# Kernel tuning notes

Hardware: AMD Instinct MI355X
Metric: run time of the kernel (lower is better)

Reference implementation:

```python
import jax, jax.numpy as jnp
import numpy as np

B, T, C, H = 4, 2048, 1024, 16
D = C // H  # head_dim = 64

def setup_inputs() -> dict:
    key = jax.random.key(0)
    k1, k2, k3 = jax.random.split(key, 3)
    x = jax.random.normal(k1, (B, T, C), dtype=jnp.float32)
    # Linear weights stored as (out_features, in_features) like torch; we apply x @ W.T
    w_attn = jax.random.normal(k2, (3 * C, C), dtype=jnp.float32) * (1.0 / np.sqrt(C))
    w_proj = jax.random.normal(k3, (C, C), dtype=jnp.float32) * (1.0 / np.sqrt(C))
    return {"x": x, "w_attn": w_attn, "w_proj": w_proj}

def reference(x, w_attn, w_proj):
    Bv, Tv, Cv = x.shape
    qkv = jnp.einsum('btc,fc->btf', x, w_attn)  # [B,T,3C]
    q, k, v = jnp.split(qkv, 3, axis=-1)
    # [B,H,T,D]
    q = q.reshape(Bv, Tv, H, D).transpose(0, 2, 1, 3)
    k = k.reshape(Bv, Tv, H, D).transpose(0, 2, 1, 3)
    v = v.reshape(Bv, Tv, H, D).transpose(0, 2, 1, 3)
    scale = 1.0 / np.sqrt(D).astype(np.float32)
    att = jnp.einsum('bhqd,bhkd->bhqk', q, k) * scale
    causal = jnp.tril(jnp.ones((Tv, Tv), dtype=bool))
    att = jnp.where(causal, att, -jnp.inf)
    att = jax.nn.softmax(att, axis=-1)
    y = jnp.einsum('bhqk,bhkd->bhqd', att, v)
    y = y.transpose(0, 2, 1, 3).reshape(Bv, Tv, Cv)
    return jnp.einsum('btc,oc->bto', y, w_proj)
```

## Files before the change

kernel.cpp:

```cpp
#include <hip/hip_runtime.h>
#include <cstdint>
#include <cstddef>

typedef __attribute__((ext_vector_type(8))) short short8;
typedef __attribute__((ext_vector_type(4))) float f32x4;
typedef unsigned int u32;

#define MFMA_BF16(a, b, c) __builtin_amdgcn_mfma_f32_16x16x32_bf16((a), (b), (c), 0, 0, 0)

__device__ __forceinline__ void async16(const void* g, void* l) {
  __builtin_amdgcn_global_load_lds(
      (const __attribute__((address_space(1))) u32*)g,
      (__attribute__((address_space(3))) u32*)l, 16, 0, 0);
}

__device__ __forceinline__ short f2bf(float f) {
  u32 u = __builtin_bit_cast(u32, f);
  u += 0x7fffu + ((u >> 16) & 1u);
  return (short)(u >> 16);
}

__device__ __forceinline__ u32 pack_bf16_trunc(float lo, float hi) {
  return __builtin_amdgcn_perm(__builtin_bit_cast(u32, hi),
                               __builtin_bit_cast(u32, lo), 0x07060302u);
}

__global__ __launch_bounds__(256) void cast_all_kernel(
    const float* __restrict__ x, const float* __restrict__ wa,
    const float* __restrict__ wp, short* __restrict__ xb,
    short* __restrict__ wab, short* __restrict__ wpb) {
  const int i = blockIdx.x * blockDim.x + threadIdx.x;
  const float4* src;
  short4* dst;
  float sc = 1.0f;
  if (i < 2097152) {
    src = (const float4*)x + i;
    dst = (short4*)xb + i;
  } else if (i < 2883584) {
    const int j = i - 2097152;
    if (j < 262144) sc = 0.18033688011112042f;
    src = (const float4*)wa + j;
    dst = (short4*)wab + j;
  } else {
    const int j = i - 2883584;
    src = (const float4*)wp + j;
    dst = (short4*)wpb + j;
  }
  float4 v = *src;
  short4 r;
  r.x = f2bf(v.x * sc); r.y = f2bf(v.y * sc);
  r.z = f2bf(v.z * sc); r.w = f2bf(v.w * sc);
  *dst = r;
}

template <bool OUT_BF16>
__global__ __launch_bounds__(256) void gemm_bt_kernel(
    const short* __restrict__ A, const short* __restrict__ Bt,
    void* __restrict__ Cv, int M, int N, int K) {
  __shared__ __align__(16) short As[128 * 64];
  __shared__ __align__(16) short Bs[128 * 64];

  const int tid  = threadIdx.x;
  const int lane = tid & 63;
  const int wave = tid >> 6;
  const int quad = lane >> 4;
  const int l15  = lane & 15;

  const int id  = blockIdx.y * gridDim.x + blockIdx.x;
  const int xcd = id & 7;
  const int j   = id >> 3;
  const int by  = xcd * 8 + (j & 7);
  const int bx  = j >> 3;
  const int bm  = by * 128;
  const int bn  = bx * 128;

  const int wm = (wave >> 1) * 64;
  const int wn = (wave & 1) * 64;

  f32x4 acc[4][4];
#pragma unroll
  for (int i = 0; i < 4; ++i)
#pragma unroll
    for (int jj = 0; jj < 4; ++jj) acc[i][jj] = (f32x4){0.f, 0.f, 0.f, 0.f};

  int srow[4], scol[4];
#pragma unroll
  for (int it = 0; it < 4; ++it) {
    const int s = tid + it * 256;
    srow[it] = s >> 3;
    scol[it] = ((s & 7) ^ (srow[it] & 7)) * 8;
  }
  const int xk = l15 & 7;

  for (int k0 = 0; k0 < K; k0 += 64) {
    __syncthreads();
#pragma unroll
    for (int it = 0; it < 4; ++it) {
      const int s = tid + it * 256;
      async16(A  + (size_t)(bm + srow[it]) * K + k0 + scol[it], &As[s * 8]);
      async16(Bt + (size_t)(bn + srow[it]) * K + k0 + scol[it], &Bs[s * 8]);
    }
    __syncthreads();

    short8 af[4][2], bf[4][2];
#pragma unroll
    for (int mt = 0; mt < 4; ++mt) {
      const int ra = (wm + mt * 16 + l15) * 64;
      af[mt][0] = *(const short8*)&As[ra + ((quad) ^ xk) * 8];
      af[mt][1] = *(const short8*)&As[ra + ((4 + quad) ^ xk) * 8];
    }
#pragma unroll
    for (int nt = 0; nt < 4; ++nt) {
      const int rb = (wn + nt * 16 + l15) * 64;
      bf[nt][0] = *(const short8*)&Bs[rb + ((quad) ^ xk) * 8];
      bf[nt][1] = *(const short8*)&Bs[rb + ((4 + quad) ^ xk) * 8];
    }
#pragma unroll
    for (int kk = 0; kk < 2; ++kk)
#pragma unroll
      for (int mt = 0; mt < 4; ++mt)
#pragma unroll
        for (int nt = 0; nt < 4; ++nt)
          acc[mt][nt] = MFMA_BF16(af[mt][kk], bf[nt][kk], acc[mt][nt]);
  }

#pragma unroll
  for (int mt = 0; mt < 4; ++mt) {
    const int r0e = bm + wm + mt * 16 + quad * 4;
#pragma unroll
    for (int nt = 0; nt < 4; ++nt) {
      const int c = bn + wn + nt * 16 + l15;
#pragma unroll
      for (int reg = 0; reg < 4; ++reg) {
        float v = acc[mt][nt][reg];
        if (OUT_BF16)
          ((short*)Cv)[(size_t)(r0e + reg) * N + c] = f2bf(v);
        else
          ((float*)Cv)[(size_t)(r0e + reg) * N + c] = v;
      }
    }
  }
}

__global__ __launch_bounds__(256) void vtrans_kernel(
    const short* __restrict__ qkv, short* __restrict__ vt2) {
  __shared__ __align__(16) short Ts[64 * 80];
  const int kt = blockIdx.x;
  const int t0 = kt * 64;
  const int bh = blockIdx.y;
  const int b = bh >> 4, h = bh & 15;
  const int tid = threadIdx.x;
#pragma unroll
  for (int it = 0; it < 2; ++it) {
    const int ci = tid + it * 256;
    const int t = ci >> 3, cw = ci & 7;
    short8 v = *(const short8*)(qkv + (size_t)(b * 2048 + t0 + t) * 3072 +
                                2048 + h * 64 + cw * 8);
    *(short8*)&Ts[t * 80 + cw * 8] = v;
  }
  __syncthreads();
#pragma unroll
  for (int it = 0; it < 2; ++it) {
    const int ci = tid + it * 256;
    const int d = ci >> 3, c2 = ci & 7;
    short tmp[8];
#pragma unroll
    for (int j = 0; j < 8; ++j) tmp[j] = Ts[(c2 * 8 + j) * 80 + d];
    short* dst = vt2 +
        (size_t)((bh * 32 + kt) * 8 + (d >> 4) * 2 + (c2 >> 2)) * 512 +
        ((c2 & 3) * 16 + (d & 15)) * 8;
    *(short8*)dst = *(short8*)tmp;
  }
}

__global__ __launch_bounds__(256, 4) void attn_kernel(
    const short* __restrict__ qkv, const short* __restrict__ vt2,
    short* __restrict__ y) {
  __shared__ __align__(16) short Ks[2][4096];
  __shared__ __align__(16) short Ps[4][1024];

  const int bh    = blockIdx.x;
  const int pairi = blockIdx.y;
  const int b = bh >> 4, h = bh & 15;
  const int tid  = threadIdx.x;
  const int lane = tid & 63;
  const int wave = tid >> 6;
  const int quad = lane >> 4, l15 = lane & 15;
  const int base_row = b * 2048;
  short* Pw = &Ps[wave][0];

  const int s0 = tid, s1 = tid + 256;
  const int r0s = s0 >> 3, c0s = (s0 & 7) ^ (r0s & 7);
  const int r1s = s1 >> 3, c1s = (s1 & 7) ^ (r1s & 7);
  const short* kbase0 = qkv + (size_t)(base_row + r0s) * 3072 + 1024 + h * 64 + c0s * 8;
  const short* kbase1 = qkv + (size_t)(base_row + r1s) * 3072 + 1024 + h * 64 + c1s * 8;

  const short* v2base = vt2 + (size_t)bh * 32 * 4096 + (size_t)lane * 8;

  const int xk = l15 & 7;

  for (int half = 0; half < 2; ++half) {
    const int qi  = half ? (31 - pairi) : pairi;
    const int nkt = qi + 1;
    const int qg0 = qi * 64 + wave * 16;

    short8 qf[2];
    {
      const short* qp = qkv +
          (size_t)(base_row + qg0 + l15) * 3072 + h * 64 + quad * 8;
      qf[0] = *(const short8*)qp;
      qf[1] = *(const short8*)(qp + 32);
    }
    float l_r = 0.f;
    f32x4 o[4];
#pragma unroll
    for (int dt = 0; dt < 4; ++dt) o[dt] = (f32x4){0.f, 0.f, 0.f, 0.f};

    async16(kbase0, &Ks[0][s0 * 8]);
    async16(kbase1, &Ks[0][s1 * 8]);

    for (int kt = 0; kt < nkt; ++kt) {
      const int kvb = kt * 64;
      __syncthreads();

      if (kt + 1 < nkt) {
        const int nb = (kt + 1) & 1;
        const size_t koff = (size_t)(kvb + 64) * 3072;
        async16(kbase0 + koff, &Ks[nb][s0 * 8]);
        async16(kbase1 + koff, &Ks[nb][s1 * 8]);
      }
      const short* Kb = &Ks[kt & 1][0];

      const short* vp = v2base + (size_t)kt * 4096;
      short8 vf[4][2];
#pragma unroll
      for (int dt = 0; dt < 4; ++dt) {
        vf[dt][0] = *(const short8*)(vp + (dt * 2 + 0) * 512);
        vf[dt][1] = *(const short8*)(vp + (dt * 2 + 1) * 512);
      }

      short8 kf[4][2];
#pragma unroll
      for (int nt = 0; nt < 4; ++nt) {
        kf[nt][0] = *(const short8*)&Kb[(nt * 16 + l15) * 64 + ((quad) ^ xk) * 8];
        kf[nt][1] = *(const short8*)&Kb[(nt * 16 + l15) * 64 + ((4 + quad) ^ xk) * 8];
      }

      f32x4 s[4];
#pragma unroll
      for (int nt = 0; nt < 4; ++nt) {
        s[nt] = MFMA_BF16(kf[nt][0], qf[0], ((f32x4){0.f, 0.f, 0.f, 0.f}));
        s[nt] = MFMA_BF16(kf[nt][1], qf[1], s[nt]);
      }

      float p[4][4];
      if (kvb + 64 <= qg0) {
#pragma unroll
        for (int nt = 0; nt < 4; ++nt)
#pragma unroll
          for (int r = 0; r < 4; ++r)
            p[nt][r] = __builtin_amdgcn_exp2f(s[nt][r]);
      } else {
        const int qrel = qg0 + l15 - kvb;
#pragma unroll
        for (int nt = 0; nt < 4; ++nt)
#pragma unroll
          for (int r = 0; r < 4; ++r) {
            const int kvl = nt * 16 + quad * 4 + r;
            p[nt][r] = (kvl <= qrel) ? __builtin_amdgcn_exp2f(s[nt][r]) : 0.f;
          }
      }

      float rs = ((p[0][0] + p[0][1]) + (p[0][2] + p[0][3])) +
                 ((p[1][0] + p[1][1]) + (p[1][2] + p[1][3])) +
                 ((p[2][0] + p[2][1]) + (p[2][2] + p[2][3])) +
                 ((p[3][0] + p[3][1]) + (p[3][2] + p[3][3]));
      rs += __shfl_xor(rs, 16);
      rs += __shfl_xor(rs, 32);
      l_r += rs;

#pragma unroll
      for (int nt = 0; nt < 4; ++nt) {
        u32 w0 = pack_bf16_trunc(p[nt][0], p[nt][1]);
        u32 w1 = pack_bf16_trunc(p[nt][2], p[nt][3]);
        const int p0 = 8 * nt + 2 * quad;
        u32* dst = (u32*)Pw + (p0 >> 4) * 256 + ((p0 >> 2) & 3) * 64 +
                   l15 * 4 + (p0 & 3);
        *(uint2*)dst = make_uint2(w0, w1);
      }
      short8 pf0 = *(const short8*)&Pw[quad * 128 + l15 * 8];
      short8 pf1 = *(const short8*)&Pw[512 + quad * 128 + l15 * 8];

#pragma unroll
      for (int dt = 0; dt < 4; ++dt) {
        o[dt] = MFMA_BF16(vf[dt][0], pf0, o[dt]);
        o[dt] = MFMA_BF16(vf[dt][1], pf1, o[dt]);
      }
    }

    {
      const float inv = 1.f / l_r;
#pragma unroll
      for (int dt = 0; dt < 4; ++dt) {
        const int d = dt * 16 + quad * 4;
        u32 w0 = pack_bf16_trunc(o[dt][0] * inv, o[dt][1] * inv);
        u32 w1 = pack_bf16_trunc(o[dt][2] * inv, o[dt][3] * inv);
        *(uint2*)&Pw[(d >> 5) * 512 + l15 * 32 + (d & 31)] = make_uint2(w0, w1);
      }
      const int qq = lane >> 2, ck = lane & 3;
      const size_t yrow = (size_t)(base_row + qg0 + qq);
#pragma unroll
      for (int kkd = 0; kkd < 2; ++kkd) {
        short8 vv = *(const short8*)&Pw[kkd * 512 + qq * 32 + ck * 8];
        *(short8*)(y + yrow * 1024 + h * 64 + kkd * 32 + ck * 8) = vv;
      }
    }
    __syncthreads();
  }
}

extern "C" void kernel_launch(void* const* d_in, const int* in_sizes, int n_in,
                              void* d_out, int out_size, void* d_ws,
                              size_t ws_size, hipStream_t stream) {
  const float* x  = (const float*)d_in[0];
  const float* wa = (const float*)d_in[1];
  const float* wp = (const float*)d_in[2];
  float* out = (float*)d_out;

  char* ws = (char*)d_ws;
  short* xb  = (short*)(ws + 0);
  short* wab = (short*)(ws + 16777216);
  short* wpb = (short*)(ws + 23068672);
  short* qkv = (short*)(ws + 25165824);
  short* yb  = (short*)(ws + 75497472);
  short* vtb = xb;

  cast_all_kernel<<<12288, 256, 0, stream>>>(x, wa, wp, xb, wab, wpb);

  gemm_bt_kernel<true><<<dim3(3072 / 128, 8192 / 128), 256, 0, stream>>>(
      xb, wab, (void*)qkv, 8192, 3072, 1024);

  vtrans_kernel<<<dim3(32, 64), 256, 0, stream>>>(qkv, vtb);

  attn_kernel<<<dim3(64, 16), 256, 0, stream>>>(qkv, vtb, yb);

  gemm_bt_kernel<false><<<dim3(1024 / 128, 8192 / 128), 256, 0, stream>>>(
      yb, wpb, (void*)out, 8192, 1024, 1024);
}
```

Before: 242.2 us.

## Fuse V transpose into QKV GEMM epilogue and drop vtrans kernel

The QKV GEMM epilogue now writes the V columns directly in the MFMA-fragment transposed layout inside the qkv buffer's V region, packing four bf16 values per 8-byte store. This removes the separate vtrans kernel launch and its extra read/write pass over V. The attention kernel reads V fragments from the re-laid-out qkv region with a 3072-element row stride. The cost is scattered 8-byte stores in the GEMM epilogue and V loads in attention that stride across rows, which may coalesce worse than the old contiguous vt2 buffer.

```diff
diff --git a/kernel.cpp b/kernel.cpp
--- a/kernel.cpp
+++ b/kernel.cpp
@@ -53,7 +53,7 @@
   *dst = r;
 }
 
-template <bool OUT_BF16>
+template <bool OUT_BF16, bool V_FUSE>
 __global__ __launch_bounds__(256) void gemm_bt_kernel(
     const short* __restrict__ A, const short* __restrict__ Bt,
     void* __restrict__ Cv, int M, int N, int K) {
@@ -124,58 +124,54 @@
           acc[mt][nt] = MFMA_BF16(af[mt][kk], bf[nt][kk], acc[mt][nt]);
   }
 
-#pragma unroll
-  for (int mt = 0; mt < 4; ++mt) {
-    const int r0e = bm + wm + mt * 16 + quad * 4;
-#pragma unroll
-    for (int nt = 0; nt < 4; ++nt) {
-      const int c = bn + wn + nt * 16 + l15;
-#pragma unroll
-      for (int reg = 0; reg < 4; ++reg) {
-        float v = acc[mt][nt][reg];
-        if (OUT_BF16)
-          ((short*)Cv)[(size_t)(r0e + reg) * N + c] = f2bf(v);
-        else
-          ((float*)Cv)[(size_t)(r0e + reg) * N + c] = v;
-      }
-    }
-  }
-}
-
-__global__ __launch_bounds__(256) void vtrans_kernel(
-    const short* __restrict__ qkv, short* __restrict__ vt2) {
-  __shared__ __align__(16) short Ts[64 * 80];
-  const int kt = blockIdx.x;
-  const int t0 = kt * 64;
-  const int bh = blockIdx.y;
-  const int b = bh >> 4, h = bh & 15;
-  const int tid = threadIdx.x;
-#pragma unroll
-  for (int it = 0; it < 2; ++it) {
-    const int ci = tid + it * 256;
-    const int t = ci >> 3, cw = ci & 7;
-    short8 v = *(const short8*)(qkv + (size_t)(b * 2048 + t0 + t) * 3072 +
-                                2048 + h * 64 + cw * 8);
-    *(short8*)&Ts[t * 80 + cw * 8] = v;
-  }
-  __syncthreads();
-#pragma unroll
-  for (int it = 0; it < 2; ++it) {
-    const int ci = tid + it * 256;
-    const int d = ci >> 3, c2 = ci & 7;
-    short tmp[8];
-#pragma unroll
-    for (int j = 0; j < 8; ++j) tmp[j] = Ts[(c2 * 8 + j) * 80 + d];
-    short* dst = vt2 +
-        (size_t)((bh * 32 + kt) * 8 + (d >> 4) * 2 + (c2 >> 2)) * 512 +
-        ((c2 & 3) * 16 + (d & 15)) * 8;
-    *(short8*)dst = *(short8*)tmp;
+  if (V_FUSE && bn >= 2048) {
+    const int b   = bm >> 11;
+    const int btt = bm & 2047;
+#pragma unroll
+    for (int mt = 0; mt < 4; ++mt) {
+      const int tt   = btt + wm + mt * 16;
+      const int kt   = tt >> 6;
+      const int t64b = (tt & 63) + quad * 4;
+      const int kkb  = t64b >> 5;
+      const int q16  = (t64b >> 3) & 3;
+      const int jb   = t64b & 7;
+#pragma unroll
+      for (int nt = 0; nt < 4; ++nt) {
+        const int dcol = bn - 2048 + wn + nt * 16;
+        const int h  = dcol >> 6;
+        const int dt = (dcol >> 4) & 3;
+        short* dst = (short*)Cv +
+            (size_t)(b * 2048 + kt * 64 + h * 4 + dt) * 3072 + 2048 +
+            kkb * 512 + (q16 * 16 + l15) * 8 + jb;
+        u32 w0 = (u32)(unsigned short)f2bf(acc[mt][nt][0]) |
+                 ((u32)(unsigned short)f2bf(acc[mt][nt][1]) << 16);
+        u32 w1 = (u32)(unsigned short)f2bf(acc[mt][nt][2]) |
+                 ((u32)(unsigned short)f2bf(acc[mt][nt][3]) << 16);
+        *(uint2*)dst = make_uint2(w0, w1);
+      }
+    }
+  } else {
+#pragma unroll
+    for (int mt = 0; mt < 4; ++mt) {
+      const int r0e = bm + wm + mt * 16 + quad * 4;
+#pragma unroll
+      for (int nt = 0; nt < 4; ++nt) {
+        const int c = bn + wn + nt * 16 + l15;
+#pragma unroll
+        for (int reg = 0; reg < 4; ++reg) {
+          float v = acc[mt][nt][reg];
+          if (OUT_BF16)
+            ((short*)Cv)[(size_t)(r0e + reg) * N + c] = f2bf(v);
+          else
+            ((float*)Cv)[(size_t)(r0e + reg) * N + c] = v;
+        }
+      }
+    }
   }
 }
 
 __global__ __launch_bounds__(256, 4) void attn_kernel(
-    const short* __restrict__ qkv, const short* __restrict__ vt2,
-    short* __restrict__ y) {
+    const short* __restrict__ qkv, short* __restrict__ y) {
   __shared__ __align__(16) short Ks[2][4096];
   __shared__ __align__(16) short Ps[4][1024];
 
@@ -195,7 +191,8 @@
   const short* kbase0 = qkv + (size_t)(base_row + r0s) * 3072 + 1024 + h * 64 + c0s * 8;
   const short* kbase1 = qkv + (size_t)(base_row + r1s) * 3072 + 1024 + h * 64 + c1s * 8;
 
-  const short* v2base = vt2 + (size_t)bh * 32 * 4096 + (size_t)lane * 8;
+  const short* vbaseA = qkv + ((size_t)base_row + h * 4) * 3072 + 2048 +
+                        (size_t)lane * 8;
 
   const int xk = l15 & 7;
 
@@ -231,12 +228,12 @@
       }
       const short* Kb = &Ks[kt & 1][0];
 
-      const short* vp = v2base + (size_t)kt * 4096;
+      const short* vp = vbaseA + (size_t)kt * 64 * 3072;
       short8 vf[4][2];
 #pragma unroll
       for (int dt = 0; dt < 4; ++dt) {
-        vf[dt][0] = *(const short8*)(vp + (dt * 2 + 0) * 512);
-        vf[dt][1] = *(const short8*)(vp + (dt * 2 + 1) * 512);
+        vf[dt][0] = *(const short8*)(vp + (size_t)dt * 3072);
+        vf[dt][1] = *(const short8*)(vp + (size_t)dt * 3072 + 512);
       }
 
       short8 kf[4][2];
@@ -333,17 +330,14 @@
   short* wpb = (short*)(ws + 23068672);
   short* qkv = (short*)(ws + 25165824);
   short* yb  = (short*)(ws + 75497472);
-  short* vtb = xb;
 
   cast_all_kernel<<<12288, 256, 0, stream>>>(x, wa, wp, xb, wab, wpb);
 
-  gemm_bt_kernel<true><<<dim3(3072 / 128, 8192 / 128), 256, 0, stream>>>(
+  gemm_bt_kernel<true, true><<<dim3(3072 / 128, 8192 / 128), 256, 0, stream>>>(
       xb, wab, (void*)qkv, 8192, 3072, 1024);
 
-  vtrans_kernel<<<dim3(32, 64), 256, 0, stream>>>(qkv, vtb);
-
-  attn_kernel<<<dim3(64, 16), 256, 0, stream>>>(qkv, vtb, yb);
-
-  gemm_bt_kernel<false><<<dim3(1024 / 128, 8192 / 128), 256, 0, stream>>>(
+  attn_kernel<<<dim3(64, 16), 256, 0, stream>>>(qkv, yb);
+
+  gemm_bt_kernel<false, false><<<dim3(1024 / 128, 8192 / 128), 256, 0, stream>>>(
       yb, wpb, (void*)out, 8192, 1024, 1024);
 }
```

Result: faster. 226.7 us (-6.4%).
